# Performance work log

Hardware: AMD Instinct MI355X
Metric: run time of the kernel (lower is better)

Reference implementation:

```python
import jax, jax.numpy as jnp
import numpy as np

N_ELEMENTS = 1_000_000
D_FEAT = 128
N_SEGMENTS = 16384


def setup_inputs() -> dict:
    key = jax.random.key(0)
    kx, ki = jax.random.split(key)
    x = jax.random.normal(kx, (N_ELEMENTS, D_FEAT), dtype=jnp.float32)
    index = jnp.sort(jax.random.randint(ki, (N_ELEMENTS,), 0, N_SEGMENTS, dtype=jnp.int64))
    return {"x": x, "index": index}


def reference(x, index):
    # scatter_add(x, index, dim=0): out[s] = sum over rows i with index[i] == s
    return jax.ops.segment_sum(x, index, num_segments=N_SEGMENTS)
```

## Files before the change

### kernel.cpp

```cpp
#include <hip/hip_runtime.h>


constexpr int D_FEAT = 128;
constexpr int D4 = D_FEAT / 4;
constexpr int ROWS_PER_WAVE = 128;
constexpr int WAVES_PER_BLOCK = 4;

__global__ void zero_out_kernel(float4* __restrict__ out, int n4) {
    int i = blockIdx.x * blockDim.x + threadIdx.x;
    int stride = gridDim.x * blockDim.x;
    for (; i < n4; i += stride) {
        out[i] = make_float4(0.f, 0.f, 0.f, 0.f);
    }
}

__device__ __forceinline__ void flush_acc(float* __restrict__ out, int seg,
                                          int cq, const float4& a) {
    float* o = out + (long)seg * D_FEAT + cq * 4;
    atomicAdd(o + 0, a.x);
    atomicAdd(o + 1, a.y);
    atomicAdd(o + 2, a.z);
    atomicAdd(o + 3, a.w);
}

__global__ __launch_bounds__(256, 8) void segsum_kernel(
        const float* __restrict__ x,
        const int* __restrict__ index,
        float* __restrict__ out,
        int n_rows) {
    const int lane = threadIdx.x & 63;
    const int half = lane >> 5;
    const int cq   = lane & 31;
    const long wave = (long)blockIdx.x * WAVES_PER_BLOCK + (threadIdx.x >> 6);

    long row0 = wave * ROWS_PER_WAVE;
    if (row0 >= n_rows) return;
    long rend = row0 + ROWS_PER_WAVE;
    if (rend > n_rows) rend = n_rows;
    const int nr = (int)(rend - row0);
    const int npairs = nr >> 1;
    const int odd = nr & 1;

    int pack = 0;
    {
        long ib = row0 + 2 * lane;
        if (ib + 1 < (long)n_rows) {
            int2 t = *(const int2*)(index + ib);
            pack = (t.x & 0xFFFF) | (t.y << 16);
        } else if (ib < (long)n_rows) {
            pack = index[ib] & 0xFFFF;
        }
    }
    const int sh = half << 4;

    int cur_seg = (__shfl(pack, 0) >> sh) & 0xFFFF;
    float4 acc = make_float4(0.f, 0.f, 0.f, 0.f);

    const float4* __restrict__ xp =
        (const float4*)x + (row0 + half) * (long)D4 + cq;

    int p = 0;
    constexpr int U = 4;
    for (; p + U <= npairs; p += U, xp += 2 * U * D4) {
        float4 v0 = xp[0 * 2 * D4];
        float4 v1 = xp[1 * 2 * D4];
        float4 v2 = xp[2 * 2 * D4];
        float4 v3 = xp[3 * 2 * D4];

        int s0 = (__shfl(pack, p + 0) >> sh) & 0xFFFF;
        if (s0 != cur_seg) { flush_acc(out, cur_seg, cq, acc); cur_seg = s0; acc = v0; }
        else { acc.x += v0.x; acc.y += v0.y; acc.z += v0.z; acc.w += v0.w; }

        int s1 = (__shfl(pack, p + 1) >> sh) & 0xFFFF;
        if (s1 != cur_seg) { flush_acc(out, cur_seg, cq, acc); cur_seg = s1; acc = v1; }
        else { acc.x += v1.x; acc.y += v1.y; acc.z += v1.z; acc.w += v1.w; }

        int s2 = (__shfl(pack, p + 2) >> sh) & 0xFFFF;
        if (s2 != cur_seg) { flush_acc(out, cur_seg, cq, acc); cur_seg = s2; acc = v2; }
        else { acc.x += v2.x; acc.y += v2.y; acc.z += v2.z; acc.w += v2.w; }

        int s3 = (__shfl(pack, p + 3) >> sh) & 0xFFFF;
        if (s3 != cur_seg) { flush_acc(out, cur_seg, cq, acc); cur_seg = s3; acc = v3; }
        else { acc.x += v3.x; acc.y += v3.y; acc.z += v3.z; acc.w += v3.w; }
    }
    for (; p < npairs; ++p, xp += 2 * D4) {
        float4 v = xp[0];
        int s = (__shfl(pack, p) >> sh) & 0xFFFF;
        if (s != cur_seg) { flush_acc(out, cur_seg, cq, acc); cur_seg = s; acc = v; }
        else { acc.x += v.x; acc.y += v.y; acc.z += v.z; acc.w += v.w; }
    }
    if (odd) {
        int s = (__shfl(pack, npairs) >> sh) & 0xFFFF;
        if (half == 0) {
            float4 v = ((const float4*)x)[(rend - 1) * (long)D4 + cq];
            if (s != cur_seg) { flush_acc(out, cur_seg, cq, acc); cur_seg = s; acc = v; }
            else { acc.x += v.x; acc.y += v.y; acc.z += v.z; acc.w += v.w; }
        }
    }

    flush_acc(out, cur_seg, cq, acc);
}

extern "C" void kernel_launch(void* const* d_in, const int* in_sizes, int n_in,
                              void* d_out, int out_size, void* d_ws, size_t ws_size,
                              hipStream_t stream) {
    const float* x = (const float*)d_in[0];
    const int* index = (const int*)d_in[1];
    float* out = (float*)d_out;

    const int n_rows = in_sizes[1];
    const int n_out4 = out_size / 4;

    zero_out_kernel<<<256, 256, 0, stream>>>((float4*)out, n_out4);

    const long n_waves = ((long)n_rows + ROWS_PER_WAVE - 1) / ROWS_PER_WAVE;
    const int n_blocks = (int)((n_waves + WAVES_PER_BLOCK - 1) / WAVES_PER_BLOCK);
    segsum_kernel<<<n_blocks, 256, 0, stream>>>(x, index, out, n_rows);
}
```

Baseline: 671.1 us.

## Assign one wave per segment via binary search, drop atomics and zero-fill

Replaces the row-chunked kernel, which flushed partial sums with float atomics into a zeroed output, with one wave per output segment. Each wave binary-searches the sorted index to find its row range, sums the rows branch-free, combines the two half-waves with a shuffle and writes the result with a plain store. This removes the zero-out kernel, all atomics and the per-row segment comparisons. In exchange each wave runs a roughly 20-step global binary search, and work per wave now depends on segment size, which can unbalance skewed inputs.

```diff
diff --git a/kernel.cpp b/kernel.cpp
--- a/kernel.cpp
+++ b/kernel.cpp
@@ -3,102 +3,64 @@
 
 constexpr int D_FEAT = 128;
 constexpr int D4 = D_FEAT / 4;
-constexpr int ROWS_PER_WAVE = 128;
 constexpr int WAVES_PER_BLOCK = 4;
 
-__global__ void zero_out_kernel(float4* __restrict__ out, int n4) {
-    int i = blockIdx.x * blockDim.x + threadIdx.x;
-    int stride = gridDim.x * blockDim.x;
-    for (; i < n4; i += stride) {
-        out[i] = make_float4(0.f, 0.f, 0.f, 0.f);
-    }
-}
-
-__device__ __forceinline__ void flush_acc(float* __restrict__ out, int seg,
-                                          int cq, const float4& a) {
-    float* o = out + (long)seg * D_FEAT + cq * 4;
-    atomicAdd(o + 0, a.x);
-    atomicAdd(o + 1, a.y);
-    atomicAdd(o + 2, a.z);
-    atomicAdd(o + 3, a.w);
-}
-
-__global__ __launch_bounds__(256, 8) void segsum_kernel(
+__global__ __launch_bounds__(256, 8) void segsum_by_segment(
         const float* __restrict__ x,
         const int* __restrict__ index,
         float* __restrict__ out,
-        int n_rows) {
+        int n_rows, int n_segments) {
     const int lane = threadIdx.x & 63;
     const int half = lane >> 5;
     const int cq   = lane & 31;
-    const long wave = (long)blockIdx.x * WAVES_PER_BLOCK + (threadIdx.x >> 6);
+    const int seg  = blockIdx.x * WAVES_PER_BLOCK + (threadIdx.x >> 6);
+    if (seg >= n_segments) return;
 
-    long row0 = wave * ROWS_PER_WAVE;
-    if (row0 >= n_rows) return;
-    long rend = row0 + ROWS_PER_WAVE;
-    if (rend > n_rows) rend = n_rows;
-    const int nr = (int)(rend - row0);
+    int target = seg + (lane & 1);
+    int lo = 0, hi = n_rows;
+    while (lo < hi) {
+        int mid = (lo + hi) >> 1;
+        if (index[mid] < target) lo = mid + 1; else hi = mid;
+    }
+    const int start = __shfl(lo, 0);
+    const int end   = __shfl(lo, 1);
+
+    const int nr     = end - start;
     const int npairs = nr >> 1;
-    const int odd = nr & 1;
 
-    int pack = 0;
-    {
-        long ib = row0 + 2 * lane;
-        if (ib + 1 < (long)n_rows) {
-            int2 t = *(const int2*)(index + ib);
-            pack = (t.x & 0xFFFF) | (t.y << 16);
-        } else if (ib < (long)n_rows) {
-            pack = index[ib] & 0xFFFF;
-        }
-    }
-    const int sh = half << 4;
-
-    int cur_seg = (__shfl(pack, 0) >> sh) & 0xFFFF;
     float4 acc = make_float4(0.f, 0.f, 0.f, 0.f);
 
     const float4* __restrict__ xp =
-        (const float4*)x + (row0 + half) * (long)D4 + cq;
+        (const float4*)x + (long)(start + half) * D4 + cq;
 
     int p = 0;
-    constexpr int U = 4;
-    for (; p + U <= npairs; p += U, xp += 2 * U * D4) {
+    for (; p + 4 <= npairs; p += 4, xp += 8 * D4) {
         float4 v0 = xp[0 * 2 * D4];
         float4 v1 = xp[1 * 2 * D4];
         float4 v2 = xp[2 * 2 * D4];
         float4 v3 = xp[3 * 2 * D4];
-
-        int s0 = (__shfl(pack, p + 0) >> sh) & 0xFFFF;
-        if (s0 != cur_seg) { flush_acc(out, cur_seg, cq, acc); cur_seg = s0; acc = v0; }
-        else { acc.x += v0.x; acc.y += v0.y; acc.z += v0.z; acc.w += v0.w; }
-
-        int s1 = (__shfl(pack, p + 1) >> sh) & 0xFFFF;
-        if (s1 != cur_seg) { flush_acc(out, cur_seg, cq, acc); cur_seg = s1; acc = v1; }
-        else { acc.x += v1.x; acc.y += v1.y; acc.z += v1.z; acc.w += v1.w; }
-
-        int s2 = (__shfl(pack, p + 2) >> sh) & 0xFFFF;
-        if (s2 != cur_seg) { flush_acc(out, cur_seg, cq, acc); cur_seg = s2; acc = v2; }
-        else { acc.x += v2.x; acc.y += v2.y; acc.z += v2.z; acc.w += v2.w; }
-
-        int s3 = (__shfl(pack, p + 3) >> sh) & 0xFFFF;
-        if (s3 != cur_seg) { flush_acc(out, cur_seg, cq, acc); cur_seg = s3; acc = v3; }
-        else { acc.x += v3.x; acc.y += v3.y; acc.z += v3.z; acc.w += v3.w; }
+        acc.x += v0.x; acc.y += v0.y; acc.z += v0.z; acc.w += v0.w;
+        acc.x += v1.x; acc.y += v1.y; acc.z += v1.z; acc.w += v1.w;
+        acc.x += v2.x; acc.y += v2.y; acc.z += v2.z; acc.w += v2.w;
+        acc.x += v3.x; acc.y += v3.y; acc.z += v3.z; acc.w += v3.w;
     }
     for (; p < npairs; ++p, xp += 2 * D4) {
         float4 v = xp[0];
-        int s = (__shfl(pack, p) >> sh) & 0xFFFF;
-        if (s != cur_seg) { flush_acc(out, cur_seg, cq, acc); cur_seg = s; acc = v; }
-        else { acc.x += v.x; acc.y += v.y; acc.z += v.z; acc.w += v.w; }
+        acc.x += v.x; acc.y += v.y; acc.z += v.z; acc.w += v.w;
     }
-    if (odd) {
-        int s = (__shfl(pack, npairs) >> sh) & 0xFFFF;
-        if (half == 0) {
-            float4 v = ((const float4*)x)[(rend - 1) * (long)D4 + cq];
-            if (s != cur_seg) { flush_acc(out, cur_seg, cq, acc); cur_seg = s; acc = v; }
-            else { acc.x += v.x; acc.y += v.y; acc.z += v.z; acc.w += v.w; }
-        }
+    if ((nr & 1) && half == 0) {
+        float4 v = ((const float4*)x)[(long)(end - 1) * D4 + cq];
+        acc.x += v.x; acc.y += v.y; acc.z += v.z; acc.w += v.w;
     }
 
-    flush_acc(out, cur_seg, cq, acc);
+    acc.x += __shfl(acc.x, lane ^ 32);
+    acc.y += __shfl(acc.y, lane ^ 32);
+    acc.z += __shfl(acc.z, lane ^ 32);
+    acc.w += __shfl(acc.w, lane ^ 32);
+
+    if (half == 0) {
+        ((float4*)out)[(long)seg * D4 + cq] = acc;
+    }
 }
 
 extern "C" void kernel_launch(void* const* d_in, const int* in_sizes, int n_in,
@@ -109,11 +71,9 @@
     float* out = (float*)d_out;
 
     const int n_rows = in_sizes[1];
-    const int n_out4 = out_size / 4;
+    const int n_segments = out_size / D_FEAT;
 
-    zero_out_kernel<<<256, 256, 0, stream>>>((float4*)out, n_out4);
-
-    const long n_waves = ((long)n_rows + ROWS_PER_WAVE - 1) / ROWS_PER_WAVE;
-    const int n_blocks = (int)((n_waves + WAVES_PER_BLOCK - 1) / WAVES_PER_BLOCK);
-    segsum_kernel<<<n_blocks, 256, 0, stream>>>(x, index, out, n_rows);
+    const int n_blocks = (n_segments + WAVES_PER_BLOCK - 1) / WAVES_PER_BLOCK;
+    segsum_by_segment<<<n_blocks, 256, 0, stream>>>(x, index, out,
+                                                    n_rows, n_segments);
 }
```

New measurement: 656.4 us. -2.2%, faster.
